# Kernel tuning notes

Hardware: AMD Instinct MI355X
Metric: run time of the kernel (lower is better)

The kernel has to match this reference:

```python
import jax, jax.numpy as jnp
import numpy as np

C_IN, C, N_HEAD = 256, 32, 8

def setup_inputs() -> dict:
    key = jax.random.key(0)
    ks = jax.random.split(key, 9)
    B, S = 4, 2048
    x = jax.random.normal(ks[0], (B, S, C_IN), dtype=jnp.float32)
    bias = jax.random.normal(ks[1], (1, N_HEAD, S, S), dtype=jnp.float32)
    s = 0.02
    Wq = jax.random.normal(ks[2], (C_IN, C * N_HEAD), dtype=jnp.float32) * s
    Wk = jax.random.normal(ks[3], (C_IN, C * N_HEAD), dtype=jnp.float32) * s
    Wv = jax.random.normal(ks[4], (C_IN, C * N_HEAD), dtype=jnp.float32) * s
    Wg = jax.random.normal(ks[5], (C_IN, C * N_HEAD), dtype=jnp.float32) * s
    bg = jnp.zeros((C * N_HEAD,), dtype=jnp.float32)
    Wo = jax.random.normal(ks[6], (C * N_HEAD, C_IN), dtype=jnp.float32) * s
    bo = jnp.zeros((C_IN,), dtype=jnp.float32)
    return {"x": x, "bias": bias, "Wq": Wq, "Wk": Wk, "Wv": Wv,
            "Wg": Wg, "bg": bg, "Wo": Wo, "bo": bo}

def reference(x, bias, Wq, Wk, Wv, Wg, bg, Wo, bo):
    B, S, _ = x.shape
    # projections (attn_dim = -2, so no movedim needed for [B, S, c_in])
    q = (x @ Wq).reshape(B, S, N_HEAD, C).transpose(0, 2, 1, 3)  # [B,H,S,C]
    k = (x @ Wk).reshape(B, S, N_HEAD, C).transpose(0, 2, 1, 3)
    v = (x @ Wv).reshape(B, S, N_HEAD, C).transpose(0, 2, 1, 3)
    q = q / jnp.sqrt(jnp.asarray(C, dtype=q.dtype))
    a = jnp.einsum('bhqc,bhkc->bhqk', q, k) + bias  # [B,H,S,S]
    a = jax.nn.softmax(a, axis=-1)
    o = jnp.einsum('bhqk,bhkc->bhqc', a, v)         # [B,H,S,C]
    o = o.transpose(0, 2, 1, 3).reshape(B, S, N_HEAD * C)
    g = jax.nn.sigmoid(x @ Wg + bg)
    o = g * o
    return o @ Wo + bo
```

## Files before the change

### kernel.cpp

```cpp
#include <hip/hip_runtime.h>

#define BB   4
#define SS   2048
#define HH   8
#define CC   32
#define CIN  256

typedef unsigned short u16;
typedef unsigned int   u32;
typedef u16 u16x4 __attribute__((ext_vector_type(4)));
typedef u16 u16x8 __attribute__((ext_vector_type(8)));
typedef __bf16 bf16x8 __attribute__((ext_vector_type(8)));
typedef float f32x4 __attribute__((ext_vector_type(4)));

__device__ __forceinline__ f32x4 mfma16(u16x8 a, u16x8 b, f32x4 c) {
  return __builtin_amdgcn_mfma_f32_16x16x32_bf16(
      __builtin_bit_cast(bf16x8, a), __builtin_bit_cast(bf16x8, b), c, 0, 0, 0);
}

__device__ __forceinline__ u32 cvtpk(float a, float b) {
  u32 r;
  asm("v_cvt_pk_bf16_f32 %0, %1, %2" : "=v"(r) : "v"(a), "v"(b));
  return r;
}

__device__ __forceinline__ f32x4 ldf4(const float* p) {
  float4 v = *(const float4*)p;
  f32x4 z = {v.x, v.y, v.z, v.w};
  return z;
}

__device__ __forceinline__ u16 bf16_rne(float x) {
  unsigned u = __float_as_uint(x);
  u += 0x7FFFu + ((u >> 16) & 1u);
  return (u16)(u >> 16);
}
__device__ __forceinline__ void cvt_pair(float x, u16 &hi, u16 &lo) {
  hi = bf16_rne(x);
  lo = bf16_rne(x - __uint_as_float(((unsigned)hi) << 16));
}

__global__ void k_cvt_x(const float* __restrict__ x,
                        u16* __restrict__ xh, u16* __restrict__ xl) {
  int i = (blockIdx.x * 256 + threadIdx.x) * 4;
  float4 v = *(const float4*)(x + i);
  u16x4 h, l;
  u16 th, tl;
  cvt_pair(v.x, th, tl); h[0] = th; l[0] = tl;
  cvt_pair(v.y, th, tl); h[1] = th; l[1] = tl;
  cvt_pair(v.z, th, tl); h[2] = th; l[2] = tl;
  cvt_pair(v.w, th, tl); h[3] = th; l[3] = tl;
  *(u16x4*)(xh + i) = h;
  *(u16x4*)(xl + i) = l;
}

__global__ void k_cvt_w(const float* __restrict__ Wq, const float* __restrict__ Wk,
                        const float* __restrict__ Wv, const float* __restrict__ Wg,
                        const float* __restrict__ Wo,
                        u16* __restrict__ wt4h, u16* __restrict__ wt4l,
                        u16* __restrict__ woth, u16* __restrict__ wotl) {
  __shared__ float tile[64][65];
  const int mat = blockIdx.x / 16, tt = blockIdx.x % 16;
  const int m0 = (tt >> 2) * 64, n0 = (tt & 3) * 64;
  const float* W = (mat == 0) ? Wq : (mat == 1) ? Wk : (mat == 2) ? Wv
                 : (mat == 3) ? Wg : Wo;
  const int tr = threadIdx.x >> 6;
  const int tc = threadIdx.x & 63;
#pragma unroll
  for (int i = 0; i < 16; ++i) {
    int row = i * 4 + tr;
    tile[row][tc] = W[(m0 + row) * 256 + n0 + tc];
  }
  __syncthreads();
  u16* dh = (mat < 4) ? wt4h : woth;
  u16* dl = (mat < 4) ? wt4l : wotl;
  const int nbase = (mat < 4) ? mat * 256 : 0;
#pragma unroll
  for (int i = 0; i < 16; ++i) {
    int row = i * 4 + tr;
    u16 hi, lo; cvt_pair(tile[tc][row], hi, lo);
    dh[(nbase + n0 + row) * 256 + m0 + tc] = hi;
    dl[(nbase + n0 + row) * 256 + m0 + tc] = lo;
  }
}

__global__ __launch_bounds__(256, 2) void k_proj(
    const u16* __restrict__ xh, const u16* __restrict__ xl,
    const u16* __restrict__ wt4h, const u16* __restrict__ wt4l,
    const float* __restrict__ bg,
    u16* __restrict__ qh, u16* __restrict__ ql,
    u16* __restrict__ kh, u16* __restrict__ kl,
    u16* __restrict__ vth, u16* __restrict__ vtl,
    float* __restrict__ g) {
  const int m0 = blockIdx.x * 128;
  const int n0 = blockIdx.y * 128;
  const int wave = threadIdx.x >> 6;
  const int lane = threadIdx.x & 63;
  const int wm = (wave >> 1) * 64, wn = (wave & 1) * 64;
  const int l15 = lane & 15, lg = lane >> 4;

  f32x4 acc[4][4] = {};
  for (int ks = 0; ks < 8; ++ks) {
    u16x8 a_h[4], a_l[4], b_h[4], b_l[4];
#pragma unroll
    for (int mt = 0; mt < 4; ++mt) {
      int base = (m0 + wm + mt * 16 + l15) * 256 + ks * 32 + lg * 8;
      a_h[mt] = *(const u16x8*)(xh + base);
      a_l[mt] = *(const u16x8*)(xl + base);
    }
#pragma unroll
    for (int nt = 0; nt < 4; ++nt) {
      int base = (n0 + wn + nt * 16 + l15) * 256 + ks * 32 + lg * 8;
      b_h[nt] = *(const u16x8*)(wt4h + base);
      b_l[nt] = *(const u16x8*)(wt4l + base);
    }
#pragma unroll
    for (int mt = 0; mt < 4; ++mt)
#pragma unroll
      for (int nt = 0; nt < 4; ++nt) {
        acc[mt][nt] = mfma16(a_h[mt], b_h[nt], acc[mt][nt]);
        acc[mt][nt] = mfma16(a_h[mt], b_l[nt], acc[mt][nt]);
        acc[mt][nt] = mfma16(a_l[mt], b_h[nt], acc[mt][nt]);
      }
  }

  const float qscale = 0.17677669529663687f;
#pragma unroll
  for (int mt = 0; mt < 4; ++mt)
#pragma unroll
    for (int nt = 0; nt < 4; ++nt) {
      const int rowb = m0 + wm + mt * 16 + lg * 4;
      const int col  = n0 + wn + nt * 16 + l15;
      const int bb = rowb >> 11, s = rowb & 2047;
      const int mid = col >> 8, d = col & 255;
      const int hh = d >> 5, c = d & 31;
      if (mid == 3) {
#pragma unroll
        for (int r = 0; r < 4; ++r) {
          float gv = 1.0f / (1.0f + __expf(-(acc[mt][nt][r] + bg[d])));
          g[(rowb + r) * 256 + d] = gv;
        }
      } else if (mid == 2) {
        u16x4 vh4, vl4;
#pragma unroll
        for (int r = 0; r < 4; ++r) {
          u16 th, tl; cvt_pair(acc[mt][nt][r], th, tl);
          vh4[r] = th; vl4[r] = tl;
        }
        size_t idx = ((size_t)(bb * HH + hh) * CC + c) * SS + s;
        *(u16x4*)(vth + idx) = vh4;
        *(u16x4*)(vtl + idx) = vl4;
      } else {
#pragma unroll
        for (int r = 0; r < 4; ++r) {
          float val = acc[mt][nt][r];
          if (mid == 0) val *= qscale;
          u16 th, tl; cvt_pair(val, th, tl);
          size_t idx = ((size_t)(bb * HH + hh) * SS + s + r) * CC + c;
          if (mid == 0) { qh[idx] = th; ql[idx] = tl; }
          else          { kh[idx] = th; kl[idx] = tl; }
        }
      }
    }
}

__global__ __launch_bounds__(256, 2) void k_attn(
    const u16* __restrict__ qh, const u16* __restrict__ ql,
    const u16* __restrict__ kh, const u16* __restrict__ kl,
    const u16* __restrict__ vth, const u16* __restrict__ vtl,
    const float* __restrict__ bias, float* __restrict__ o) {
  __shared__ __align__(16) u32 lds32[19968];
  u16* ldsu = (u16*)lds32;

  const int idx  = blockIdx.x;
  const int h    = idx & 7;
  const int b    = (idx >> 3) & 3;
  const int q0   = (idx >> 5) * 128;
  const int w    = threadIdx.x >> 6;
  const int lane = threadIdx.x & 63;
  const int l15 = lane & 15, lg = lane >> 4;
  const int bh = b * HH + h;
  const int t = threadIdx.x;

  const int kj = t >> 2, kc = (t & 3) * 8;
  const int vc = t >> 3, vj = (t & 7) * 8;
  const size_t gkbase = ((size_t)bh * SS + kj) * CC + kc;
  const size_t gvbase = ((size_t)bh * CC + vc) * SS + vj;

  u16x8 qfh[2], qfl[2];
#pragma unroll
  for (int qt = 0; qt < 2; ++qt) {
    int base = (bh * SS + q0 + w * 32 + qt * 16 + l15) * CC + lg * 8;
    qfh[qt] = *(const u16x8*)(qh + base);
    qfl[qt] = *(const u16x8*)(ql + base);
  }

  const float* biasQ[2];
#pragma unroll
  for (int qt = 0; qt < 2; ++qt)
    biasQ[qt] = bias + (size_t)h * SS * SS
              + (size_t)(q0 + w * 32 + qt * 16 + l15) * SS + lg * 4;

  u32* pw = lds32 + 10752 + w * 2304;

  f32x4 oacc[2][2] = {};
  float rs[2] = {0.0f, 0.0f};

  u16x8 skh, skl, svh, svl;
  skh = *(const u16x8*)(kh + gkbase);
  skl = *(const u16x8*)(kl + gkbase);
  svh = *(const u16x8*)(vth + gvbase);
  svl = *(const u16x8*)(vtl + gvbase);
  f32x4 bcur[2][4];
#pragma unroll
  for (int qt = 0; qt < 2; ++qt)
#pragma unroll
    for (int at = 0; at < 4; ++at)
      bcur[qt][at] = ldf4(biasQ[qt] + at * 16);
  *(u16x8*)(ldsu + kj * 40 + kc) = skh;
  *(u16x8*)(ldsu + 2560 + kj * 40 + kc) = skl;
  *(u16x8*)(ldsu + 5120 + vc * 88 + vj) = svh;
  *(u16x8*)(ldsu + 7936 + vc * 88 + vj) = svl;
  __syncthreads();

#pragma unroll 1
  for (int jt = 0; jt < 32; ++jt) {
    const int cur = jt & 1;
    const u16* lk = ldsu + cur * 10752;

    if (jt < 31) {
      const size_t joff = (size_t)(jt + 1) * 64;
      skh = *(const u16x8*)(kh + gkbase + joff * CC);
      skl = *(const u16x8*)(kl + gkbase + joff * CC);
      svh = *(const u16x8*)(vth + gvbase + joff);
      svl = *(const u16x8*)(vtl + gvbase + joff);
    }
    f32x4 bnxt[2][4];
    if (jt < 31) {
#pragma unroll
      for (int qt = 0; qt < 2; ++qt)
#pragma unroll
        for (int at = 0; at < 4; ++at)
          bnxt[qt][at] = ldf4(biasQ[qt] + (jt + 1) * 64 + at * 16);
    }

    u16x8 ka_h[4], ka_l[4];
#pragma unroll
    for (int at = 0; at < 4; ++at) {
      int base = (at * 16 + l15) * 40 + lg * 8;
      ka_h[at] = *(const u16x8*)(lk + base);
      ka_l[at] = *(const u16x8*)(lk + 2560 + base);
    }
    f32x4 sacc[2][4];
#pragma unroll
    for (int qt = 0; qt < 2; ++qt)
#pragma unroll
      for (int at = 0; at < 4; ++at)
        sacc[qt][at] = bcur[qt][at];
#pragma unroll
    for (int at = 0; at < 4; ++at)
#pragma unroll
      for (int qt = 0; qt < 2; ++qt) {
        sacc[qt][at] = mfma16(ka_h[at], qfh[qt], sacc[qt][at]);
        sacc[qt][at] = mfma16(ka_h[at], qfl[qt], sacc[qt][at]);
        sacc[qt][at] = mfma16(ka_l[at], qfh[qt], sacc[qt][at]);
      }
#pragma unroll
    for (int qt = 0; qt < 2; ++qt) {
      u32* pq = pw + qt * 1152;
#pragma unroll
      for (int at = 0; at < 4; ++at) {
        float p0 = __expf(sacc[qt][at][0]);
        float p1 = __expf(sacc[qt][at][1]);
        float p2 = __expf(sacc[qt][at][2]);
        float p3 = __expf(sacc[qt][at][3]);
        rs[qt] += (p0 + p1) + (p2 + p3);
        u32 hA = cvtpk(p0, p1), hB = cvtpk(p2, p3);
        float f0 = __uint_as_float(hA << 16);
        float f1 = __uint_as_float(hA & 0xffff0000u);
        float f2 = __uint_as_float(hB << 16);
        float f3 = __uint_as_float(hB & 0xffff0000u);
        u32 lA = cvtpk(p0 - f0, p1 - f1);
        u32 lB = cvtpk(p2 - f2, p3 - f3);
        int off = l15 * 36 + 8 * at + 2 * lg;
        uint2 Hv; Hv.x = hA; Hv.y = hB;
        uint2 Lv; Lv.x = lA; Lv.y = lB;
        *(uint2*)&pq[off] = Hv;
        *(uint2*)&pq[off + 576] = Lv;
      }
    }
#pragma unroll
    for (int ks = 0; ks < 2; ++ks) {
      int roff = l15 * 36 + 16 * ks + 4 * lg;
      u16x8 pa_h[2], pa_l[2];
#pragma unroll
      for (int qt = 0; qt < 2; ++qt) {
        pa_h[qt] = *(const u16x8*)(pw + qt * 1152 + roff);
        pa_l[qt] = *(const u16x8*)(pw + qt * 1152 + 576 + roff);
      }
#pragma unroll
      for (int ct = 0; ct < 2; ++ct) {
        int voff = (ct * 16 + l15) * 88 + ks * 32 + lg * 8;
        u16x8 vfh = *(const u16x8*)(lk + 5120 + voff);
        u16x8 vfl = *(const u16x8*)(lk + 7936 + voff);
#pragma unroll
        for (int qt = 0; qt < 2; ++qt) {
          oacc[qt][ct] = mfma16(pa_h[qt], vfh, oacc[qt][ct]);
          oacc[qt][ct] = mfma16(pa_h[qt], vfl, oacc[qt][ct]);
          oacc[qt][ct] = mfma16(pa_l[qt], vfh, oacc[qt][ct]);
        }
      }
    }
    if (jt < 31) {
      u16* ln = ldsu + (cur ^ 1) * 10752;
      *(u16x8*)(ln + kj * 40 + kc) = skh;
      *(u16x8*)(ln + 2560 + kj * 40 + kc) = skl;
      *(u16x8*)(ln + 5120 + vc * 88 + vj) = svh;
      *(u16x8*)(ln + 7936 + vc * 88 + vj) = svl;
#pragma unroll
      for (int qt = 0; qt < 2; ++qt)
#pragma unroll
        for (int at = 0; at < 4; ++at)
          bcur[qt][at] = bnxt[qt][at];
    }
    __syncthreads();
  }

#pragma unroll
  for (int qt = 0; qt < 2; ++qt) {
    rs[qt] += __shfl_xor(rs[qt], 16, 64);
    rs[qt] += __shfl_xor(rs[qt], 32, 64);
  }
#pragma unroll
  for (int qt = 0; qt < 2; ++qt) {
    float rsT[4];
#pragma unroll
    for (int r = 0; r < 4; ++r) rsT[r] = __shfl(rs[qt], lg * 4 + r, 64);
#pragma unroll
    for (int ct = 0; ct < 2; ++ct)
#pragma unroll
      for (int r = 0; r < 4; ++r) {
        int qg = q0 + w * 32 + qt * 16 + lg * 4 + r;
        o[((size_t)(b * SS + qg) * HH + h) * CC + ct * 16 + l15] =
            oacc[qt][ct][r] / rsT[r];
      }
  }
}

__global__ __launch_bounds__(256, 2) void k_out(
    const float* __restrict__ o, const float* __restrict__ g,
    const u16* __restrict__ woth, const u16* __restrict__ wotl,
    const float* __restrict__ bo, float* __restrict__ out) {
  const int m0 = blockIdx.x * 32;
  const int n0 = blockIdx.y * 128;
  const int wave = threadIdx.x >> 6;
  const int lane = threadIdx.x & 63;
  const int wn = wave * 32;
  const int l15 = lane & 15, lg = lane >> 4;

  f32x4 acc[2][2] = {};
  for (int ks = 0; ks < 8; ++ks) {
    u16x8 a_h[2], a_l[2], b_h[2], b_l[2];
#pragma unroll
    for (int mt = 0; mt < 2; ++mt) {
      int base = (m0 + mt * 16 + l15) * 256 + ks * 32 + lg * 8;
      float4 o0 = *(const float4*)(o + base);
      float4 o1 = *(const float4*)(o + base + 4);
      float4 g0 = *(const float4*)(g + base);
      float4 g1 = *(const float4*)(g + base + 4);
      float pr[8] = {o0.x * g0.x, o0.y * g0.y, o0.z * g0.z, o0.w * g0.w,
                     o1.x * g1.x, o1.y * g1.y, o1.z * g1.z, o1.w * g1.w};
      union { u16 s[8]; u16x8 v; } uh, ul;
#pragma unroll
      for (int e = 0; e < 8; ++e) { u16 th, tl; cvt_pair(pr[e], th, tl); uh.s[e] = th; ul.s[e] = tl; }
      a_h[mt] = uh.v; a_l[mt] = ul.v;
    }
#pragma unroll
    for (int nt = 0; nt < 2; ++nt) {
      int base = (n0 + wn + nt * 16 + l15) * 256 + ks * 32 + lg * 8;
      b_h[nt] = *(const u16x8*)(woth + base);
      b_l[nt] = *(const u16x8*)(wotl + base);
    }
#pragma unroll
    for (int mt = 0; mt < 2; ++mt)
#pragma unroll
      for (int nt = 0; nt < 2; ++nt) {
        acc[mt][nt] = mfma16(a_h[mt], b_h[nt], acc[mt][nt]);
        acc[mt][nt] = mfma16(a_h[mt], b_l[nt], acc[mt][nt]);
        acc[mt][nt] = mfma16(a_l[mt], b_h[nt], acc[mt][nt]);
      }
  }
#pragma unroll
  for (int mt = 0; mt < 2; ++mt)
#pragma unroll
    for (int nt = 0; nt < 2; ++nt)
#pragma unroll
      for (int r = 0; r < 4; ++r) {
        int row = m0 + mt * 16 + lg * 4 + r;
        int col = n0 + wn + nt * 16 + l15;
        out[row * 256 + col] = acc[mt][nt][r] + bo[col];
      }
}

extern "C" void kernel_launch(void* const* d_in, const int* in_sizes, int n_in,
                              void* d_out, int out_size, void* d_ws, size_t ws_size,
                              hipStream_t stream) {
  const float* x    = (const float*)d_in[0];
  const float* bias = (const float*)d_in[1];
  const float* Wq   = (const float*)d_in[2];
  const float* Wk   = (const float*)d_in[3];
  const float* Wv   = (const float*)d_in[4];
  const float* Wg   = (const float*)d_in[5];
  const float* bg   = (const float*)d_in[6];
  const float* Wo   = (const float*)d_in[7];
  const float* bo   = (const float*)d_in[8];
  float* out = (float*)d_out;

  char* p = (char*)d_ws;
  size_t used = 0;
  auto alloc = [&](size_t bytes) -> void* {
    void* r = p + used;
    used += (bytes + 255) & ~(size_t)255;
    return r;
  };
  const size_t NTOK = (size_t)BB * SS * CIN;
  u16* xh   = (u16*)alloc(NTOK * 2);
  u16* xl   = (u16*)alloc(NTOK * 2);
  u16* wt4h = (u16*)alloc(1024 * 256 * 2);
  u16* wt4l = (u16*)alloc(1024 * 256 * 2);
  u16* woth = (u16*)alloc(256 * 256 * 2);
  u16* wotl = (u16*)alloc(256 * 256 * 2);
  u16* qh   = (u16*)alloc(NTOK * 2);
  u16* ql   = (u16*)alloc(NTOK * 2);
  u16* kh   = (u16*)alloc(NTOK * 2);
  u16* kl   = (u16*)alloc(NTOK * 2);
  u16* vth  = (u16*)alloc(NTOK * 2);
  u16* vtl  = (u16*)alloc(NTOK * 2);
  float* gbuf = (float*)alloc(NTOK * 4);
  float* obuf = (float*)alloc(NTOK * 4);
  if (used > ws_size) return;

  k_cvt_x<<<dim3(2048), dim3(256), 0, stream>>>(x, xh, xl);
  k_cvt_w<<<dim3(80), dim3(256), 0, stream>>>(Wq, Wk, Wv, Wg, Wo, wt4h, wt4l, woth, wotl);
  k_proj<<<dim3(64, 8), dim3(256), 0, stream>>>(xh, xl, wt4h, wt4l, bg,
                                                qh, ql, kh, kl, vth, vtl, gbuf);
  k_attn<<<dim3(512), dim3(256), 0, stream>>>(qh, ql, kh, kl, vth, vtl, bias, obuf);
  k_out<<<dim3(256, 2), dim3(256), 0, stream>>>(obuf, gbuf, woth, wotl, bo, out);
}
```

Baseline: 164.1 us.

## Split attention keys across two blocks and keep P in registers via 16x16x16 MFMA

Attention now splits the key range into two halves, so twice as many blocks run. Each half writes an unnormalized numerator and a row-sum, and the output kernel combines them, normalizes and applies the gate. The P matrix no longer goes through LDS: the score accumulator layout is fed straight into 16x16x16 bf16 MFMAs. This lowers LDS use and raises the occupancy target to 4. Bias loads are no longer prefetched a tile ahead, and the extra partial buffers add global traffic in the output kernel.

```diff
diff --git a/kernel.cpp b/kernel.cpp
--- a/kernel.cpp
+++ b/kernel.cpp
@@ -10,12 +10,26 @@
 typedef unsigned int   u32;
 typedef u16 u16x4 __attribute__((ext_vector_type(4)));
 typedef u16 u16x8 __attribute__((ext_vector_type(8)));
+typedef u32 u32x2 __attribute__((ext_vector_type(2)));
+typedef short s16x4 __attribute__((ext_vector_type(4)));
 typedef __bf16 bf16x8 __attribute__((ext_vector_type(8)));
 typedef float f32x4 __attribute__((ext_vector_type(4)));
 
 __device__ __forceinline__ f32x4 mfma16(u16x8 a, u16x8 b, f32x4 c) {
   return __builtin_amdgcn_mfma_f32_16x16x32_bf16(
       __builtin_bit_cast(bf16x8, a), __builtin_bit_cast(bf16x8, b), c, 0, 0, 0);
+}
+
+__device__ __forceinline__ f32x4 mfma16k(u32x2 a, u32x2 b, f32x4 c) {
+#if __has_builtin(__builtin_amdgcn_mfma_f32_16x16x16bf16_1k)
+  return __builtin_amdgcn_mfma_f32_16x16x16bf16_1k(
+      __builtin_bit_cast(s16x4, a), __builtin_bit_cast(s16x4, b), c, 0, 0, 0);
+#else
+  f32x4 d = c;
+  asm volatile("v_mfma_f32_16x16x16_bf16 %0, %1, %2, %0"
+               : "+v"(d) : "v"(a), "v"(b));
+  return d;
+#endif
 }
 
 __device__ __forceinline__ u32 cvtpk(float a, float b) {
@@ -164,28 +178,35 @@
     }
 }
 
-__global__ __launch_bounds__(256, 2) void k_attn(
+__global__ __launch_bounds__(256, 4) void k_attn(
     const u16* __restrict__ qh, const u16* __restrict__ ql,
     const u16* __restrict__ kh, const u16* __restrict__ kl,
     const u16* __restrict__ vth, const u16* __restrict__ vtl,
-    const float* __restrict__ bias, float* __restrict__ o) {
-  __shared__ __align__(16) u32 lds32[19968];
+    const float* __restrict__ bias,
+    float* __restrict__ n0, float* __restrict__ n1,
+    float* __restrict__ d0, float* __restrict__ d1) {
+  __shared__ __align__(16) u32 lds32[9728];
   u16* ldsu = (u16*)lds32;
 
-  const int idx  = blockIdx.x;
-  const int h    = idx & 7;
-  const int b    = (idx >> 3) & 3;
-  const int q0   = (idx >> 5) * 128;
+  const int idx = blockIdx.x;
+  const int h   = idx & 7;
+  const int b   = (idx >> 3) & 3;
+  const int jh  = (idx >> 5) & 1;
+  const int q0  = (idx >> 6) * 128;
   const int w    = threadIdx.x >> 6;
   const int lane = threadIdx.x & 63;
   const int l15 = lane & 15, lg = lane >> 4;
   const int bh = b * HH + h;
   const int t = threadIdx.x;
+  const int jbase = jh * 1024;
+
+  float* nb = jh ? n1 : n0;
+  float* db = jh ? d1 : d0;
 
   const int kj = t >> 2, kc = (t & 3) * 8;
   const int vc = t >> 3, vj = (t & 7) * 8;
-  const size_t gkbase = ((size_t)bh * SS + kj) * CC + kc;
-  const size_t gvbase = ((size_t)bh * CC + vc) * SS + vj;
+  const size_t gk = ((size_t)bh * SS + jbase + kj) * CC + kc;
+  const size_t gv = ((size_t)bh * CC + vc) * SS + jbase + vj;
 
   u16x8 qfh[2], qfl[2];
 #pragma unroll
@@ -199,77 +220,63 @@
 #pragma unroll
   for (int qt = 0; qt < 2; ++qt)
     biasQ[qt] = bias + (size_t)h * SS * SS
-              + (size_t)(q0 + w * 32 + qt * 16 + l15) * SS + lg * 4;
-
-  u32* pw = lds32 + 10752 + w * 2304;
+              + (size_t)(q0 + w * 32 + qt * 16 + l15) * SS + jbase + lg * 4;
 
   f32x4 oacc[2][2] = {};
   float rs[2] = {0.0f, 0.0f};
 
-  u16x8 skh, skl, svh, svl;
-  skh = *(const u16x8*)(kh + gkbase);
-  skl = *(const u16x8*)(kl + gkbase);
-  svh = *(const u16x8*)(vth + gvbase);
-  svl = *(const u16x8*)(vtl + gvbase);
-  f32x4 bcur[2][4];
-#pragma unroll
-  for (int qt = 0; qt < 2; ++qt)
-#pragma unroll
-    for (int at = 0; at < 4; ++at)
-      bcur[qt][at] = ldf4(biasQ[qt] + at * 16);
-  *(u16x8*)(ldsu + kj * 40 + kc) = skh;
-  *(u16x8*)(ldsu + 2560 + kj * 40 + kc) = skl;
-  *(u16x8*)(ldsu + 5120 + vc * 88 + vj) = svh;
-  *(u16x8*)(ldsu + 7936 + vc * 88 + vj) = svl;
+  {
+    u16x8 a = *(const u16x8*)(kh + gk);
+    u16x8 c = *(const u16x8*)(kl + gk);
+    u16x8 e = *(const u16x8*)(vth + gv);
+    u16x8 f = *(const u16x8*)(vtl + gv);
+    *(u16x8*)(ldsu + kj * 40 + kc) = a;
+    *(u16x8*)(ldsu + 2560 + kj * 40 + kc) = c;
+    *(u16x8*)(ldsu + 5120 + vc * 72 + vj) = e;
+    *(u16x8*)(ldsu + 7424 + vc * 72 + vj) = f;
+  }
   __syncthreads();
 
 #pragma unroll 1
-  for (int jt = 0; jt < 32; ++jt) {
+  for (int jt = 0; jt < 16; ++jt) {
     const int cur = jt & 1;
-    const u16* lk = ldsu + cur * 10752;
-
-    if (jt < 31) {
-      const size_t joff = (size_t)(jt + 1) * 64;
-      skh = *(const u16x8*)(kh + gkbase + joff * CC);
-      skl = *(const u16x8*)(kl + gkbase + joff * CC);
-      svh = *(const u16x8*)(vth + gvbase + joff);
-      svl = *(const u16x8*)(vtl + gvbase + joff);
-    }
-    f32x4 bnxt[2][4];
-    if (jt < 31) {
-#pragma unroll
-      for (int qt = 0; qt < 2; ++qt)
-#pragma unroll
-        for (int at = 0; at < 4; ++at)
-          bnxt[qt][at] = ldf4(biasQ[qt] + (jt + 1) * 64 + at * 16);
-    }
-
-    u16x8 ka_h[4], ka_l[4];
+    const u16* lk = ldsu + cur * 9728;
+
+    f32x4 sacc[2][4];
+#pragma unroll
+    for (int qt = 0; qt < 2; ++qt)
+#pragma unroll
+      for (int at = 0; at < 4; ++at)
+        sacc[qt][at] = ldf4(biasQ[qt] + jt * 64 + at * 16);
+
 #pragma unroll
     for (int at = 0; at < 4; ++at) {
-      int base = (at * 16 + l15) * 40 + lg * 8;
-      ka_h[at] = *(const u16x8*)(lk + base);
-      ka_l[at] = *(const u16x8*)(lk + 2560 + base);
-    }
-    f32x4 sacc[2][4];
-#pragma unroll
-    for (int qt = 0; qt < 2; ++qt)
-#pragma unroll
-      for (int at = 0; at < 4; ++at)
-        sacc[qt][at] = bcur[qt][at];
-#pragma unroll
-    for (int at = 0; at < 4; ++at)
+      int kb = (at * 16 + l15) * 40 + lg * 8;
+      u16x8 kah = *(const u16x8*)(lk + kb);
+      u16x8 kal = *(const u16x8*)(lk + 2560 + kb);
 #pragma unroll
       for (int qt = 0; qt < 2; ++qt) {
-        sacc[qt][at] = mfma16(ka_h[at], qfh[qt], sacc[qt][at]);
-        sacc[qt][at] = mfma16(ka_h[at], qfl[qt], sacc[qt][at]);
-        sacc[qt][at] = mfma16(ka_l[at], qfh[qt], sacc[qt][at]);
-      }
-#pragma unroll
-    for (int qt = 0; qt < 2; ++qt) {
-      u32* pq = pw + qt * 1152;
-#pragma unroll
-      for (int at = 0; at < 4; ++at) {
+        sacc[qt][at] = mfma16(kah, qfh[qt], sacc[qt][at]);
+        sacc[qt][at] = mfma16(kah, qfl[qt], sacc[qt][at]);
+        sacc[qt][at] = mfma16(kal, qfh[qt], sacc[qt][at]);
+      }
+    }
+
+    u16x8 skh, skl, svh, svl;
+    if (jt < 15) {
+      const size_t ko = (size_t)(jt + 1) * 64 * CC;
+      const size_t vo = (size_t)(jt + 1) * 64;
+      skh = *(const u16x8*)(kh + gk + ko);
+      skl = *(const u16x8*)(kl + gk + ko);
+      svh = *(const u16x8*)(vth + gv + vo);
+      svl = *(const u16x8*)(vtl + gv + vo);
+    }
+
+#pragma unroll
+    for (int at = 0; at < 4; ++at) {
+      u32x2 ph[2], pl[2];
+#pragma unroll
+      for (int qt = 0; qt < 2; ++qt) {
         float p0 = __expf(sacc[qt][at][0]);
         float p1 = __expf(sacc[qt][at][1]);
         float p2 = __expf(sacc[qt][at][2]);
@@ -282,46 +289,29 @@
         float f3 = __uint_as_float(hB & 0xffff0000u);
         u32 lA = cvtpk(p0 - f0, p1 - f1);
         u32 lB = cvtpk(p2 - f2, p3 - f3);
-        int off = l15 * 36 + 8 * at + 2 * lg;
-        uint2 Hv; Hv.x = hA; Hv.y = hB;
-        uint2 Lv; Lv.x = lA; Lv.y = lB;
-        *(uint2*)&pq[off] = Hv;
-        *(uint2*)&pq[off + 576] = Lv;
-      }
-    }
-#pragma unroll
-    for (int ks = 0; ks < 2; ++ks) {
-      int roff = l15 * 36 + 16 * ks + 4 * lg;
-      u16x8 pa_h[2], pa_l[2];
-#pragma unroll
-      for (int qt = 0; qt < 2; ++qt) {
-        pa_h[qt] = *(const u16x8*)(pw + qt * 1152 + roff);
-        pa_l[qt] = *(const u16x8*)(pw + qt * 1152 + 576 + roff);
+        ph[qt][0] = hA; ph[qt][1] = hB;
+        pl[qt][0] = lA; pl[qt][1] = lB;
       }
 #pragma unroll
       for (int ct = 0; ct < 2; ++ct) {
-        int voff = (ct * 16 + l15) * 88 + ks * 32 + lg * 8;
-        u16x8 vfh = *(const u16x8*)(lk + 5120 + voff);
-        u16x8 vfl = *(const u16x8*)(lk + 7936 + voff);
+        int vb = 5120 + (ct * 16 + l15) * 72 + at * 16 + lg * 4;
+        u32x2 vfh = *(const u32x2*)(lk + vb);
+        u32x2 vfl = *(const u32x2*)(lk + vb + 2304);
 #pragma unroll
         for (int qt = 0; qt < 2; ++qt) {
-          oacc[qt][ct] = mfma16(pa_h[qt], vfh, oacc[qt][ct]);
-          oacc[qt][ct] = mfma16(pa_h[qt], vfl, oacc[qt][ct]);
-          oacc[qt][ct] = mfma16(pa_l[qt], vfh, oacc[qt][ct]);
+          oacc[qt][ct] = mfma16k(ph[qt], vfh, oacc[qt][ct]);
+          oacc[qt][ct] = mfma16k(ph[qt], vfl, oacc[qt][ct]);
+          oacc[qt][ct] = mfma16k(pl[qt], vfh, oacc[qt][ct]);
         }
       }
     }
-    if (jt < 31) {
-      u16* ln = ldsu + (cur ^ 1) * 10752;
+
+    if (jt < 15) {
+      u16* ln = ldsu + (cur ^ 1) * 9728;
       *(u16x8*)(ln + kj * 40 + kc) = skh;
       *(u16x8*)(ln + 2560 + kj * 40 + kc) = skl;
-      *(u16x8*)(ln + 5120 + vc * 88 + vj) = svh;
-      *(u16x8*)(ln + 7936 + vc * 88 + vj) = svl;
-#pragma unroll
-      for (int qt = 0; qt < 2; ++qt)
-#pragma unroll
-        for (int at = 0; at < 4; ++at)
-          bcur[qt][at] = bnxt[qt][at];
+      *(u16x8*)(ln + 5120 + vc * 72 + vj) = svh;
+      *(u16x8*)(ln + 7424 + vc * 72 + vj) = svl;
     }
     __syncthreads();
   }
@@ -333,26 +323,27 @@
   }
 #pragma unroll
   for (int qt = 0; qt < 2; ++qt) {
-    float rsT[4];
-#pragma unroll
-    for (int r = 0; r < 4; ++r) rsT[r] = __shfl(rs[qt], lg * 4 + r, 64);
+    if (lg == 0)
+      db[(size_t)(b * SS + q0 + w * 32 + qt * 16 + l15) * HH + h] = rs[qt];
 #pragma unroll
     for (int ct = 0; ct < 2; ++ct)
 #pragma unroll
       for (int r = 0; r < 4; ++r) {
         int qg = q0 + w * 32 + qt * 16 + lg * 4 + r;
-        o[((size_t)(b * SS + qg) * HH + h) * CC + ct * 16 + l15] =
-            oacc[qt][ct][r] / rsT[r];
+        nb[((size_t)(b * SS + qg) * HH + h) * CC + ct * 16 + l15] =
+            oacc[qt][ct][r];
       }
   }
 }
 
 __global__ __launch_bounds__(256, 2) void k_out(
-    const float* __restrict__ o, const float* __restrict__ g,
+    const float* __restrict__ n0, const float* __restrict__ n1,
+    const float* __restrict__ d0, const float* __restrict__ d1,
+    const float* __restrict__ g,
     const u16* __restrict__ woth, const u16* __restrict__ wotl,
     const float* __restrict__ bo, float* __restrict__ out) {
   const int m0 = blockIdx.x * 32;
-  const int n0 = blockIdx.y * 128;
+  const int nn0 = blockIdx.y * 128;
   const int wave = threadIdx.x >> 6;
   const int lane = threadIdx.x & 63;
   const int wn = wave * 32;
@@ -363,13 +354,19 @@
     u16x8 a_h[2], a_l[2], b_h[2], b_l[2];
 #pragma unroll
     for (int mt = 0; mt < 2; ++mt) {
-      int base = (m0 + mt * 16 + l15) * 256 + ks * 32 + lg * 8;
-      float4 o0 = *(const float4*)(o + base);
-      float4 o1 = *(const float4*)(o + base + 4);
+      int row = m0 + mt * 16 + l15;
+      int base = row * 256 + ks * 32 + lg * 8;
+      float inv = 1.0f / (d0[row * 8 + ks] + d1[row * 8 + ks]);
+      float4 a0 = *(const float4*)(n0 + base);
+      float4 a1 = *(const float4*)(n0 + base + 4);
+      float4 c0 = *(const float4*)(n1 + base);
+      float4 c1 = *(const float4*)(n1 + base + 4);
       float4 g0 = *(const float4*)(g + base);
       float4 g1 = *(const float4*)(g + base + 4);
-      float pr[8] = {o0.x * g0.x, o0.y * g0.y, o0.z * g0.z, o0.w * g0.w,
-                     o1.x * g1.x, o1.y * g1.y, o1.z * g1.z, o1.w * g1.w};
+      float pr[8] = {(a0.x + c0.x) * inv * g0.x, (a0.y + c0.y) * inv * g0.y,
+                     (a0.z + c0.z) * inv * g0.z, (a0.w + c0.w) * inv * g0.w,
+                     (a1.x + c1.x) * inv * g1.x, (a1.y + c1.y) * inv * g1.y,
+                     (a1.z + c1.z) * inv * g1.z, (a1.w + c1.w) * inv * g1.w};
       union { u16 s[8]; u16x8 v; } uh, ul;
 #pragma unroll
       for (int e = 0; e < 8; ++e) { u16 th, tl; cvt_pair(pr[e], th, tl); uh.s[e] = th; ul.s[e] = tl; }
@@ -377,7 +374,7 @@
     }
 #pragma unroll
     for (int nt = 0; nt < 2; ++nt) {
-      int base = (n0 + wn + nt * 16 + l15) * 256 + ks * 32 + lg * 8;
+      int base = (nn0 + wn + nt * 16 + l15) * 256 + ks * 32 + lg * 8;
       b_h[nt] = *(const u16x8*)(woth + base);
       b_l[nt] = *(const u16x8*)(wotl + base);
     }
@@ -397,7 +394,7 @@
 #pragma unroll
       for (int r = 0; r < 4; ++r) {
         int row = m0 + mt * 16 + lg * 4 + r;
-        int col = n0 + wn + nt * 16 + l15;
+        int col = nn0 + wn + nt * 16 + l15;
         out[row * 256 + col] = acc[mt][nt][r] + bo[col];
       }
 }
@@ -437,13 +434,18 @@
   u16* vth  = (u16*)alloc(NTOK * 2);
   u16* vtl  = (u16*)alloc(NTOK * 2);
   float* gbuf = (float*)alloc(NTOK * 4);
-  float* obuf = (float*)alloc(NTOK * 4);
+  float* nb0  = (float*)alloc(NTOK * 4);
+  float* nb1  = (float*)alloc(NTOK * 4);
+  float* db0  = (float*)alloc((size_t)BB * SS * HH * 4);
+  float* db1  = (float*)alloc((size_t)BB * SS * HH * 4);
   if (used > ws_size) return;
 
   k_cvt_x<<<dim3(2048), dim3(256), 0, stream>>>(x, xh, xl);
   k_cvt_w<<<dim3(80), dim3(256), 0, stream>>>(Wq, Wk, Wv, Wg, Wo, wt4h, wt4l, woth, wotl);
   k_proj<<<dim3(64, 8), dim3(256), 0, stream>>>(xh, xl, wt4h, wt4l, bg,
                                                 qh, ql, kh, kl, vth, vtl, gbuf);
-  k_attn<<<dim3(512), dim3(256), 0, stream>>>(qh, ql, kh, kl, vth, vtl, bias, obuf);
-  k_out<<<dim3(256, 2), dim3(256), 0, stream>>>(obuf, gbuf, woth, wotl, bo, out);
-}
+  k_attn<<<dim3(1024), dim3(256), 0, stream>>>(qh, ql, kh, kl, vth, vtl, bias,
+                                               nb0, nb1, db0, db1);
+  k_out<<<dim3(256, 2), dim3(256), 0, stream>>>(nb0, nb1, db0, db1, gbuf,
+                                                woth, wotl, bo, out);
+}
```

Measured after the change: 175.1 us. 6.7% more time.

## Share bias tiles across two batches and split keys across blocks

Applied to the files above, without the earlier changes.

Each attention block now handles two batch elements for the same head and query tile, so every bias tile loaded from global memory serves two score computations, halving bias traffic. The key range is split in half across blocks, with each writing unnormalized partial numerators and row sums. The output kernel combines the two partials and normalizes. This relies on the softmax having no max subtraction, so the halves add directly. The cost is extra workspace, extra partial-result writes and reads, and more registers for the doubled accumulators.

```diff
diff --git a/kernel.cpp b/kernel.cpp
--- a/kernel.cpp
+++ b/kernel.cpp
@@ -12,6 +12,7 @@
 typedef u16 u16x8 __attribute__((ext_vector_type(8)));
 typedef __bf16 bf16x8 __attribute__((ext_vector_type(8)));
 typedef float f32x4 __attribute__((ext_vector_type(4)));
+
 
 __device__ __forceinline__ f32x4 mfma16(u16x8 a, u16x8 b, f32x4 c) {
   return __builtin_amdgcn_mfma_f32_16x16x32_bf16(
@@ -168,191 +169,218 @@
     const u16* __restrict__ qh, const u16* __restrict__ ql,
     const u16* __restrict__ kh, const u16* __restrict__ kl,
     const u16* __restrict__ vth, const u16* __restrict__ vtl,
-    const float* __restrict__ bias, float* __restrict__ o) {
+    const float* __restrict__ bias,
+    float* __restrict__ n0, float* __restrict__ n1,
+    float* __restrict__ d0, float* __restrict__ d1) {
   __shared__ __align__(16) u32 lds32[19968];
   u16* ldsu = (u16*)lds32;
 
-  const int idx  = blockIdx.x;
-  const int h    = idx & 7;
-  const int b    = (idx >> 3) & 3;
-  const int q0   = (idx >> 5) * 128;
+  const int idx = blockIdx.x;
+  const int h   = idx & 7;
+  const int js  = (idx >> 3) & 1;
+  const int bp  = (idx >> 4) & 1;
+  const int q0  = (idx >> 5) * 128;
   const int w    = threadIdx.x >> 6;
   const int lane = threadIdx.x & 63;
   const int l15 = lane & 15, lg = lane >> 4;
-  const int bh = b * HH + h;
   const int t = threadIdx.x;
+  const int jbase = js * 1024;
+
+  float* nbuf = js ? n1 : n0;
+  float* dbuf = js ? d1 : d0;
 
   const int kj = t >> 2, kc = (t & 3) * 8;
   const int vc = t >> 3, vj = (t & 7) * 8;
-  const size_t gkbase = ((size_t)bh * SS + kj) * CC + kc;
-  const size_t gvbase = ((size_t)bh * CC + vc) * SS + vj;
-
-  u16x8 qfh[2], qfl[2];
-#pragma unroll
-  for (int qt = 0; qt < 2; ++qt) {
-    int base = (bh * SS + q0 + w * 32 + qt * 16 + l15) * CC + lg * 8;
-    qfh[qt] = *(const u16x8*)(qh + base);
-    qfl[qt] = *(const u16x8*)(ql + base);
-  }
+  size_t kb[2], vb[2];
+#pragma unroll
+  for (int b2 = 0; b2 < 2; ++b2) {
+    const int bh2 = (bp * 2 + b2) * HH + h;
+    kb[b2] = ((size_t)bh2 * SS + jbase + kj) * CC + kc;
+    vb[b2] = ((size_t)bh2 * CC + vc) * SS + jbase + vj;
+  }
+
+  u16x8 qfh[2][2], qfl[2][2];
+#pragma unroll
+  for (int b2 = 0; b2 < 2; ++b2)
+#pragma unroll
+    for (int qt = 0; qt < 2; ++qt) {
+      int base = (((bp * 2 + b2) * HH + h) * SS + q0 + w * 32 + qt * 16 + l15)
+                 * CC + lg * 8;
+      qfh[b2][qt] = *(const u16x8*)(qh + base);
+      qfl[b2][qt] = *(const u16x8*)(ql + base);
+    }
 
   const float* biasQ[2];
 #pragma unroll
   for (int qt = 0; qt < 2; ++qt)
     biasQ[qt] = bias + (size_t)h * SS * SS
-              + (size_t)(q0 + w * 32 + qt * 16 + l15) * SS + lg * 4;
+              + (size_t)(q0 + w * 32 + qt * 16 + l15) * SS + jbase + lg * 4;
 
   u32* pw = lds32 + 10752 + w * 2304;
 
-  f32x4 oacc[2][2] = {};
-  float rs[2] = {0.0f, 0.0f};
-
-  u16x8 skh, skl, svh, svl;
-  skh = *(const u16x8*)(kh + gkbase);
-  skl = *(const u16x8*)(kl + gkbase);
-  svh = *(const u16x8*)(vth + gvbase);
-  svl = *(const u16x8*)(vtl + gvbase);
+  f32x4 oacc[2][2][2] = {};
+  float rs[2][2] = {};
+
   f32x4 bcur[2][4];
-#pragma unroll
-  for (int qt = 0; qt < 2; ++qt)
-#pragma unroll
-    for (int at = 0; at < 4; ++at)
-      bcur[qt][at] = ldf4(biasQ[qt] + at * 16);
-  *(u16x8*)(ldsu + kj * 40 + kc) = skh;
-  *(u16x8*)(ldsu + 2560 + kj * 40 + kc) = skl;
-  *(u16x8*)(ldsu + 5120 + vc * 88 + vj) = svh;
-  *(u16x8*)(ldsu + 7936 + vc * 88 + vj) = svl;
+  {
+    u16x8 a = *(const u16x8*)(kh + kb[0]);
+    u16x8 c = *(const u16x8*)(kl + kb[0]);
+    u16x8 e = *(const u16x8*)(vth + vb[0]);
+    u16x8 f = *(const u16x8*)(vtl + vb[0]);
+#pragma unroll
+    for (int qt = 0; qt < 2; ++qt)
+#pragma unroll
+      for (int at = 0; at < 4; ++at)
+        bcur[qt][at] = ldf4(biasQ[qt] + at * 16);
+    *(u16x8*)(ldsu + kj * 40 + kc) = a;
+    *(u16x8*)(ldsu + 2560 + kj * 40 + kc) = c;
+    *(u16x8*)(ldsu + 5120 + vc * 88 + vj) = e;
+    *(u16x8*)(ldsu + 7936 + vc * 88 + vj) = f;
+  }
   __syncthreads();
 
 #pragma unroll 1
-  for (int jt = 0; jt < 32; ++jt) {
-    const int cur = jt & 1;
-    const u16* lk = ldsu + cur * 10752;
-
-    if (jt < 31) {
-      const size_t joff = (size_t)(jt + 1) * 64;
-      skh = *(const u16x8*)(kh + gkbase + joff * CC);
-      skl = *(const u16x8*)(kl + gkbase + joff * CC);
-      svh = *(const u16x8*)(vth + gvbase + joff);
-      svl = *(const u16x8*)(vtl + gvbase + joff);
-    }
-    f32x4 bnxt[2][4];
-    if (jt < 31) {
+  for (int jt = 0; jt < 16; ++jt) {
+#pragma unroll
+    for (int b2 = 0; b2 < 2; ++b2) {
+      const u16* lk = ldsu + b2 * 10752;
+      u16* ln = ldsu + (b2 ^ 1) * 10752;
+      const bool hasNext = (b2 == 0) || (jt < 15);
+      const int njt = (b2 == 0) ? jt : jt + 1;
+      const int nb2 = b2 ^ 1;
+
+      u16x8 skh, skl, svh, svl;
+      if (hasNext) {
+        size_t gk = kb[nb2] + (size_t)njt * 64 * CC;
+        size_t gv = vb[nb2] + (size_t)njt * 64;
+        skh = *(const u16x8*)(kh + gk);
+        skl = *(const u16x8*)(kl + gk);
+        svh = *(const u16x8*)(vth + gv);
+        svl = *(const u16x8*)(vtl + gv);
+      }
+      f32x4 bnxt[2][4];
+      if (b2 == 1 && jt < 15) {
+#pragma unroll
+        for (int qt = 0; qt < 2; ++qt)
+#pragma unroll
+          for (int at = 0; at < 4; ++at)
+            bnxt[qt][at] = ldf4(biasQ[qt] + (jt + 1) * 64 + at * 16);
+      }
+
+      u16x8 ka_h[4], ka_l[4];
+#pragma unroll
+      for (int at = 0; at < 4; ++at) {
+        int base = (at * 16 + l15) * 40 + lg * 8;
+        ka_h[at] = *(const u16x8*)(lk + base);
+        ka_l[at] = *(const u16x8*)(lk + 2560 + base);
+      }
+      f32x4 sacc[2][4];
 #pragma unroll
       for (int qt = 0; qt < 2; ++qt)
 #pragma unroll
         for (int at = 0; at < 4; ++at)
-          bnxt[qt][at] = ldf4(biasQ[qt] + (jt + 1) * 64 + at * 16);
-    }
-
-    u16x8 ka_h[4], ka_l[4];
-#pragma unroll
-    for (int at = 0; at < 4; ++at) {
-      int base = (at * 16 + l15) * 40 + lg * 8;
-      ka_h[at] = *(const u16x8*)(lk + base);
-      ka_l[at] = *(const u16x8*)(lk + 2560 + base);
-    }
-    f32x4 sacc[2][4];
-#pragma unroll
-    for (int qt = 0; qt < 2; ++qt)
+          sacc[qt][at] = bcur[qt][at];
 #pragma unroll
       for (int at = 0; at < 4; ++at)
-        sacc[qt][at] = bcur[qt][at];
-#pragma unroll
-    for (int at = 0; at < 4; ++at)
+#pragma unroll
+        for (int qt = 0; qt < 2; ++qt) {
+          sacc[qt][at] = mfma16(ka_h[at], qfh[b2][qt], sacc[qt][at]);
+          sacc[qt][at] = mfma16(ka_h[at], qfl[b2][qt], sacc[qt][at]);
+          sacc[qt][at] = mfma16(ka_l[at], qfh[b2][qt], sacc[qt][at]);
+        }
 #pragma unroll
       for (int qt = 0; qt < 2; ++qt) {
-        sacc[qt][at] = mfma16(ka_h[at], qfh[qt], sacc[qt][at]);
-        sacc[qt][at] = mfma16(ka_h[at], qfl[qt], sacc[qt][at]);
-        sacc[qt][at] = mfma16(ka_l[at], qfh[qt], sacc[qt][at]);
-      }
+        u32* pq = pw + qt * 1152;
+#pragma unroll
+        for (int at = 0; at < 4; ++at) {
+          float p0 = __expf(sacc[qt][at][0]);
+          float p1 = __expf(sacc[qt][at][1]);
+          float p2 = __expf(sacc[qt][at][2]);
+          float p3 = __expf(sacc[qt][at][3]);
+          rs[b2][qt] += (p0 + p1) + (p2 + p3);
+          u32 hA = cvtpk(p0, p1), hB = cvtpk(p2, p3);
+          float f0 = __uint_as_float(hA << 16);
+          float f1 = __uint_as_float(hA & 0xffff0000u);
+          float f2 = __uint_as_float(hB << 16);
+          float f3 = __uint_as_float(hB & 0xffff0000u);
+          u32 lA = cvtpk(p0 - f0, p1 - f1);
+          u32 lB = cvtpk(p2 - f2, p3 - f3);
+          int off = l15 * 36 + 8 * at + 2 * lg;
+          uint2 Hv; Hv.x = hA; Hv.y = hB;
+          uint2 Lv; Lv.x = lA; Lv.y = lB;
+          *(uint2*)&pq[off] = Hv;
+          *(uint2*)&pq[off + 576] = Lv;
+        }
+      }
+#pragma unroll
+      for (int ks = 0; ks < 2; ++ks) {
+        int roff = l15 * 36 + 16 * ks + 4 * lg;
+        u16x8 pa_h[2], pa_l[2];
+#pragma unroll
+        for (int qt = 0; qt < 2; ++qt) {
+          pa_h[qt] = *(const u16x8*)(pw + qt * 1152 + roff);
+          pa_l[qt] = *(const u16x8*)(pw + qt * 1152 + 576 + roff);
+        }
+#pragma unroll
+        for (int ct = 0; ct < 2; ++ct) {
+          int voff = (ct * 16 + l15) * 88 + ks * 32 + lg * 8;
+          u16x8 vfh = *(const u16x8*)(lk + 5120 + voff);
+          u16x8 vfl = *(const u16x8*)(lk + 7936 + voff);
+#pragma unroll
+          for (int qt = 0; qt < 2; ++qt) {
+            oacc[b2][qt][ct] = mfma16(pa_h[qt], vfh, oacc[b2][qt][ct]);
+            oacc[b2][qt][ct] = mfma16(pa_h[qt], vfl, oacc[b2][qt][ct]);
+            oacc[b2][qt][ct] = mfma16(pa_l[qt], vfh, oacc[b2][qt][ct]);
+          }
+        }
+      }
+      if (hasNext) {
+        *(u16x8*)(ln + kj * 40 + kc) = skh;
+        *(u16x8*)(ln + 2560 + kj * 40 + kc) = skl;
+        *(u16x8*)(ln + 5120 + vc * 88 + vj) = svh;
+        *(u16x8*)(ln + 7936 + vc * 88 + vj) = svl;
+      }
+      if (b2 == 1 && jt < 15) {
+#pragma unroll
+        for (int qt = 0; qt < 2; ++qt)
+#pragma unroll
+          for (int at = 0; at < 4; ++at)
+            bcur[qt][at] = bnxt[qt][at];
+      }
+      __syncthreads();
+    }
+  }
+
+#pragma unroll
+  for (int b2 = 0; b2 < 2; ++b2) {
+    const int bfull = bp * 2 + b2;
 #pragma unroll
     for (int qt = 0; qt < 2; ++qt) {
-      u32* pq = pw + qt * 1152;
-#pragma unroll
-      for (int at = 0; at < 4; ++at) {
-        float p0 = __expf(sacc[qt][at][0]);
-        float p1 = __expf(sacc[qt][at][1]);
-        float p2 = __expf(sacc[qt][at][2]);
-        float p3 = __expf(sacc[qt][at][3]);
-        rs[qt] += (p0 + p1) + (p2 + p3);
-        u32 hA = cvtpk(p0, p1), hB = cvtpk(p2, p3);
-        float f0 = __uint_as_float(hA << 16);
-        float f1 = __uint_as_float(hA & 0xffff0000u);
-        float f2 = __uint_as_float(hB << 16);
-        float f3 = __uint_as_float(hB & 0xffff0000u);
-        u32 lA = cvtpk(p0 - f0, p1 - f1);
-        u32 lB = cvtpk(p2 - f2, p3 - f3);
-        int off = l15 * 36 + 8 * at + 2 * lg;
-        uint2 Hv; Hv.x = hA; Hv.y = hB;
-        uint2 Lv; Lv.x = lA; Lv.y = lB;
-        *(uint2*)&pq[off] = Hv;
-        *(uint2*)&pq[off + 576] = Lv;
-      }
-    }
-#pragma unroll
-    for (int ks = 0; ks < 2; ++ks) {
-      int roff = l15 * 36 + 16 * ks + 4 * lg;
-      u16x8 pa_h[2], pa_l[2];
-#pragma unroll
-      for (int qt = 0; qt < 2; ++qt) {
-        pa_h[qt] = *(const u16x8*)(pw + qt * 1152 + roff);
-        pa_l[qt] = *(const u16x8*)(pw + qt * 1152 + 576 + roff);
-      }
-#pragma unroll
-      for (int ct = 0; ct < 2; ++ct) {
-        int voff = (ct * 16 + l15) * 88 + ks * 32 + lg * 8;
-        u16x8 vfh = *(const u16x8*)(lk + 5120 + voff);
-        u16x8 vfl = *(const u16x8*)(lk + 7936 + voff);
-#pragma unroll
-        for (int qt = 0; qt < 2; ++qt) {
-          oacc[qt][ct] = mfma16(pa_h[qt], vfh, oacc[qt][ct]);
-          oacc[qt][ct] = mfma16(pa_h[qt], vfl, oacc[qt][ct]);
-          oacc[qt][ct] = mfma16(pa_l[qt], vfh, oacc[qt][ct]);
-        }
-      }
-    }
-    if (jt < 31) {
-      u16* ln = ldsu + (cur ^ 1) * 10752;
-      *(u16x8*)(ln + kj * 40 + kc) = skh;
-      *(u16x8*)(ln + 2560 + kj * 40 + kc) = skl;
-      *(u16x8*)(ln + 5120 + vc * 88 + vj) = svh;
-      *(u16x8*)(ln + 7936 + vc * 88 + vj) = svl;
-#pragma unroll
-      for (int qt = 0; qt < 2; ++qt)
-#pragma unroll
-        for (int at = 0; at < 4; ++at)
-          bcur[qt][at] = bnxt[qt][at];
-    }
-    __syncthreads();
-  }
-
-#pragma unroll
-  for (int qt = 0; qt < 2; ++qt) {
-    rs[qt] += __shfl_xor(rs[qt], 16, 64);
-    rs[qt] += __shfl_xor(rs[qt], 32, 64);
-  }
-#pragma unroll
-  for (int qt = 0; qt < 2; ++qt) {
-    float rsT[4];
-#pragma unroll
-    for (int r = 0; r < 4; ++r) rsT[r] = __shfl(rs[qt], lg * 4 + r, 64);
-#pragma unroll
-    for (int ct = 0; ct < 2; ++ct)
-#pragma unroll
-      for (int r = 0; r < 4; ++r) {
-        int qg = q0 + w * 32 + qt * 16 + lg * 4 + r;
-        o[((size_t)(b * SS + qg) * HH + h) * CC + ct * 16 + l15] =
-            oacc[qt][ct][r] / rsT[r];
-      }
+      rs[b2][qt] += __shfl_xor(rs[b2][qt], 16, 64);
+      rs[b2][qt] += __shfl_xor(rs[b2][qt], 32, 64);
+      if (lg == 0)
+        dbuf[(size_t)(bfull * SS + q0 + w * 32 + qt * 16 + l15) * HH + h] =
+            rs[b2][qt];
+#pragma unroll
+      for (int ct = 0; ct < 2; ++ct)
+#pragma unroll
+        for (int r = 0; r < 4; ++r) {
+          int qg = q0 + w * 32 + qt * 16 + lg * 4 + r;
+          nbuf[((size_t)(bfull * SS + qg) * HH + h) * CC + ct * 16 + l15] =
+              oacc[b2][qt][ct][r];
+        }
+    }
   }
 }
 
 __global__ __launch_bounds__(256, 2) void k_out(
-    const float* __restrict__ o, const float* __restrict__ g,
+    const float* __restrict__ n0, const float* __restrict__ n1,
+    const float* __restrict__ d0, const float* __restrict__ d1,
+    const float* __restrict__ g,
     const u16* __restrict__ woth, const u16* __restrict__ wotl,
     const float* __restrict__ bo, float* __restrict__ out) {
   const int m0 = blockIdx.x * 32;
-  const int n0 = blockIdx.y * 128;
+  const int nn0 = blockIdx.y * 128;
   const int wave = threadIdx.x >> 6;
   const int lane = threadIdx.x & 63;
   const int wn = wave * 32;
@@ -363,13 +391,19 @@
     u16x8 a_h[2], a_l[2], b_h[2], b_l[2];
 #pragma unroll
     for (int mt = 0; mt < 2; ++mt) {
-      int base = (m0 + mt * 16 + l15) * 256 + ks * 32 + lg * 8;
-      float4 o0 = *(const float4*)(o + base);
-      float4 o1 = *(const float4*)(o + base + 4);
+      int row = m0 + mt * 16 + l15;
+      int base = row * 256 + ks * 32 + lg * 8;
+      float inv = 1.0f / (d0[row * 8 + ks] + d1[row * 8 + ks]);
+      float4 a0 = *(const float4*)(n0 + base);
+      float4 a1 = *(const float4*)(n0 + base + 4);
+      float4 c0 = *(const float4*)(n1 + base);
+      float4 c1 = *(const float4*)(n1 + base + 4);
       float4 g0 = *(const float4*)(g + base);
       float4 g1 = *(const float4*)(g + base + 4);
-      float pr[8] = {o0.x * g0.x, o0.y * g0.y, o0.z * g0.z, o0.w * g0.w,
-                     o1.x * g1.x, o1.y * g1.y, o1.z * g1.z, o1.w * g1.w};
+      float pr[8] = {(a0.x + c0.x) * inv * g0.x, (a0.y + c0.y) * inv * g0.y,
+                     (a0.z + c0.z) * inv * g0.z, (a0.w + c0.w) * inv * g0.w,
+                     (a1.x + c1.x) * inv * g1.x, (a1.y + c1.y) * inv * g1.y,
+                     (a1.z + c1.z) * inv * g1.z, (a1.w + c1.w) * inv * g1.w};
       union { u16 s[8]; u16x8 v; } uh, ul;
 #pragma unroll
       for (int e = 0; e < 8; ++e) { u16 th, tl; cvt_pair(pr[e], th, tl); uh.s[e] = th; ul.s[e] = tl; }
@@ -377,7 +411,7 @@
     }
 #pragma unroll
     for (int nt = 0; nt < 2; ++nt) {
-      int base = (n0 + wn + nt * 16 + l15) * 256 + ks * 32 + lg * 8;
+      int base = (nn0 + wn + nt * 16 + l15) * 256 + ks * 32 + lg * 8;
       b_h[nt] = *(const u16x8*)(woth + base);
       b_l[nt] = *(const u16x8*)(wotl + base);
     }
@@ -397,7 +431,7 @@
 #pragma unroll
       for (int r = 0; r < 4; ++r) {
         int row = m0 + mt * 16 + lg * 4 + r;
-        int col = n0 + wn + nt * 16 + l15;
+        int col = nn0 + wn + nt * 16 + l15;
         out[row * 256 + col] = acc[mt][nt][r] + bo[col];
       }
 }
@@ -437,13 +471,18 @@
   u16* vth  = (u16*)alloc(NTOK * 2);
   u16* vtl  = (u16*)alloc(NTOK * 2);
   float* gbuf = (float*)alloc(NTOK * 4);
-  float* obuf = (float*)alloc(NTOK * 4);
+  float* nb0  = (float*)alloc(NTOK * 4);
+  float* nb1  = (float*)alloc(NTOK * 4);
+  float* db0  = (float*)alloc((size_t)BB * SS * HH * 4);
+  float* db1  = (float*)alloc((size_t)BB * SS * HH * 4);
   if (used > ws_size) return;
 
   k_cvt_x<<<dim3(2048), dim3(256), 0, stream>>>(x, xh, xl);
   k_cvt_w<<<dim3(80), dim3(256), 0, stream>>>(Wq, Wk, Wv, Wg, Wo, wt4h, wt4l, woth, wotl);
   k_proj<<<dim3(64, 8), dim3(256), 0, stream>>>(xh, xl, wt4h, wt4l, bg,
                                                 qh, ql, kh, kl, vth, vtl, gbuf);
-  k_attn<<<dim3(512), dim3(256), 0, stream>>>(qh, ql, kh, kl, vth, vtl, bias, obuf);
-  k_out<<<dim3(256, 2), dim3(256), 0, stream>>>(obuf, gbuf, woth, wotl, bo, out);
-}
+  k_attn<<<dim3(512), dim3(256), 0, stream>>>(qh, ql, kh, kl, vth, vtl, bias,
+                                              nb0, nb1, db0, db1);
+  k_out<<<dim3(256, 2), dim3(256), 0, stream>>>(nb0, nb1, db0, db1, gbuf,
+                                                woth, wotl, bo, out);
+}
```

Result: no change. 166.5 us (+1.5%).
